# Performance work log

Hardware: AMD Instinct MI355X
Metric: run time of the kernel (lower is better)

## Reference

```python
import jax, jax.numpy as jnp
import numpy as np

THETA = 10000.0

def apply_rope(x, positions):
    # x: [B, H, S, d_k], positions: [S] int
    d_k = x.shape[-1]
    inv_freq = THETA ** (-jnp.arange(0, d_k, 2, dtype=jnp.float32) / d_k)  # [d_k/2]
    ang = positions.astype(jnp.float32)[:, None] * inv_freq[None, :]        # [S, d_k/2]
    cos, sin = jnp.cos(ang), jnp.sin(ang)
    x_even = x[..., 0::2]
    x_odd = x[..., 1::2]
    r_even = x_even * cos - x_odd * sin
    r_odd = x_even * sin + x_odd * cos
    # interleave back
    return jnp.stack([r_even, r_odd], axis=-1).reshape(x.shape)

def setup_inputs() -> dict:
    key = jax.random.key(0)
    k1, k2, k3 = jax.random.split(key, 3)
    B, S, D = 2, 2048, 1024
    x = jax.random.normal(k1, (B, S, D), dtype=jnp.float32)
    token_positions = jnp.arange(S, dtype=jnp.int32)
    W_qkv = jax.random.normal(k2, (3 * D, D), dtype=jnp.float32) * 0.02
    W_o = jax.random.normal(k3, (D, D), dtype=jnp.float32) * 0.02
    return {"x": x, "token_positions": token_positions, "W_qkv": W_qkv, "W_o": W_o}

def reference(x, token_positions, W_qkv, W_o):
    B, S, D = x.shape
    H = 16
    d_k = D // H
    qkv = jnp.einsum('bsd,ed->bse', x, W_qkv)           # [B, S, 3D]
    q, k, v = jnp.split(qkv, 3, axis=-1)
    def to_heads(t):
        return t.reshape(B, S, H, d_k).transpose(0, 2, 1, 3)  # [B, H, S, d_k]
    hq, hk, hv = to_heads(q), to_heads(k), to_heads(v)
    hq = apply_rope(hq, token_positions)
    hk = apply_rope(hk, token_positions)
    scale = d_k ** -0.5
    scores = jnp.einsum('bhqd,bhkd->bhqk', hq, hk) * scale  # [B, H, S, S]
    causal = jnp.tril(jnp.ones((S, S), dtype=bool))
    scores = jnp.where(causal, scores, -jnp.inf)
    attn = jax.nn.softmax(scores, axis=-1)
    out = jnp.einsum('bhqk,bhkd->bhqd', attn, hv)           # [B, H, S, d_k]
    out = out.transpose(0, 2, 1, 3).reshape(B, S, D)
    return jnp.einsum('bsd,ed->bse', out, W_o)
```

## Files before the change

### kernel.cpp

```cpp
#include <hip/hip_runtime.h>
#include <math.h>

typedef short short8 __attribute__((ext_vector_type(8)));
typedef float f32x4 __attribute__((ext_vector_type(4)));

typedef __attribute__((address_space(1))) const void* as1p;
typedef __attribute__((address_space(3))) void* as3p;

__device__ __forceinline__ unsigned short f2bf(float f) {
    unsigned int u = __float_as_uint(f);
    u += 0x7fffu + ((u >> 16) & 1u);
    return (unsigned short)(u >> 16);
}
__device__ __forceinline__ float bf2f(unsigned int bits) {
    return __uint_as_float(bits << 16);
}

__global__ void cvt_all_bf16(const float* __restrict__ x,
                             const float* __restrict__ wqkv,
                             const float* __restrict__ wo,
                             unsigned short* __restrict__ xb,
                             unsigned short* __restrict__ wqkvb,
                             unsigned short* __restrict__ wob) {
    int i = blockIdx.x * blockDim.x + threadIdx.x;
    const float* src;
    unsigned short* dst;
    int off;
    if (i < 1048576)       { src = x;    dst = xb;    off = i; }
    else if (i < 1835008)  { src = wqkv; dst = wqkvb; off = i - 1048576; }
    else                   { src = wo;   dst = wob;   off = i - 1835008; }
    float4 v = ((const float4*)src)[off];
    ushort4 o = make_ushort4(f2bf(v.x), f2bf(v.y), f2bf(v.z), f2bf(v.w));
    ((ushort4*)dst)[off] = o;
}

template <int RF, bool BF16_OUT>
__global__ __launch_bounds__(256) void gemm_nt_mfma(
    const unsigned short* __restrict__ A, const unsigned short* __restrict__ B,
    void* __restrict__ Cv, int N, int K) {
    constexpr int BM = RF * 32;
    __shared__ unsigned short As[BM * 32];
    __shared__ unsigned short Bs[128 * 32];
    const int tid = threadIdx.x;
    const int wave = tid >> 6, lane = tid & 63;
    const int m0 = blockIdx.y * BM, n0 = blockIdx.x << 7;
    const int wr = ((wave >> 1) & 1) * (RF * 16);
    const int wc = (wave & 1) << 6;

    const int r0 = tid >> 2, ko = (tid & 3) << 3;
    const unsigned short* Ap0 = A + (size_t)(m0 + r0) * K + ko;
    const unsigned short* Ap1 = A + (size_t)(m0 + (RF == 4 ? 64 : 0) + r0) * K + ko;
    const unsigned short* Bp0 = B + (size_t)(n0 + r0) * K + ko;
    const unsigned short* Bp1 = B + (size_t)(n0 + 64 + r0) * K + ko;

    f32x4 acc[RF][4] = {};
    const int lro = lane & 15, g8 = (lane >> 4) << 3;

    for (int k0 = 0; k0 < K; k0 += 32) {
        __syncthreads();
        __builtin_amdgcn_global_load_lds((as1p)(Ap0 + k0), (as3p)(As + tid * 8), 16, 0, 0);
        if constexpr (RF == 4)
            __builtin_amdgcn_global_load_lds((as1p)(Ap1 + k0), (as3p)(As + (256 + tid) * 8), 16, 0, 0);
        __builtin_amdgcn_global_load_lds((as1p)(Bp0 + k0), (as3p)(Bs + tid * 8), 16, 0, 0);
        __builtin_amdgcn_global_load_lds((as1p)(Bp1 + k0), (as3p)(Bs + (256 + tid) * 8), 16, 0, 0);
        __syncthreads();

        short8 af[RF], bfr[4];
        #pragma unroll
        for (int i = 0; i < RF; i++) af[i] = *(const short8*)&As[(wr + i * 16 + lro) * 32 + g8];
        #pragma unroll
        for (int j = 0; j < 4; j++) bfr[j] = *(const short8*)&Bs[(wc + j * 16 + lro) * 32 + g8];
        #pragma unroll
        for (int i = 0; i < RF; i++)
            #pragma unroll
            for (int j = 0; j < 4; j++)
                acc[i][j] = __builtin_amdgcn_mfma_f32_16x16x32_bf16(af[i], bfr[j], acc[i][j], 0, 0, 0);
    }

    const int row_b = m0 + wr + ((lane >> 4) << 2);
    const int col_b = n0 + wc + lro;
    #pragma unroll
    for (int i = 0; i < RF; i++)
        #pragma unroll
        for (int j = 0; j < 4; j++)
            #pragma unroll
            for (int r = 0; r < 4; r++) {
                size_t idx = (size_t)(row_b + i * 16 + r) * N + (col_b + j * 16);
                if constexpr (BF16_OUT) ((unsigned short*)Cv)[idx] = f2bf(acc[i][j][r]);
                else ((float*)Cv)[idx] = acc[i][j][r];
            }
}

__global__ void rope_bf16(unsigned short* __restrict__ qkv,
                          const int* __restrict__ pos) {
    int p = blockIdx.x * blockDim.x + threadIdx.x;
    if (p >= 4194304) return;
    int t = p >> 10, r2 = p & 1023;
    int sec = r2 >> 9, e2 = r2 & 511;
    int hh = e2 >> 5, i = e2 & 31;
    int s = t & 2047;
    float fpos = (float)pos[s];
    float ang = fpos * exp2f(-(float)i * 0.41524101186092029f);
    float scl = (sec == 0) ? 0.18033688011112042f : 1.0f;
    float c = cosf(ang) * scl, sn = sinf(ang) * scl;
    unsigned int* base = (unsigned int*)(qkv + (size_t)t * 3072 + sec * 1024 + hh * 64 + 2 * i);
    unsigned int w = *base;
    float xe = bf2f(w & 0xffffu), xo = bf2f(w >> 16);
    float re = xe * c - xo * sn;
    float ro = xe * sn + xo * c;
    *base = (unsigned int)f2bf(re) | ((unsigned int)f2bf(ro) << 16);
}

__global__ __launch_bounds__(256) void flash_attn_mfma(
    const unsigned short* __restrict__ qkv, unsigned short* __restrict__ Ows) {
    const int S = 2048, D3 = 3072;
    const int pp = blockIdx.x, h = blockIdx.y, b = blockIdx.z;
    const int tid = threadIdx.x, wave = tid >> 6, lane = tid & 63;
    const int lro = lane & 15, grp = lane >> 4;

    __shared__ __align__(16) unsigned short Qs[64 * 64];
    __shared__ __align__(16) unsigned short Ks[2][64 * 64];
    __shared__ __align__(16) unsigned int   Vp[2][64 * 36];
    __shared__ __align__(16) unsigned short Ps[64 * 80];

    const int sr = tid >> 3;
    const int sc = ((tid & 7) ^ (sr & 7)) << 3;
    const int kp = tid >> 3, vo = (tid & 7) << 3;
    const int vka = (kp >> 1) + ((kp & 1) << 5);
    const int vcol = (((kp >> 2) ^ (tid & 7)) << 2) | (kp & 3);

    const int cq = grp ^ (lro & 7);
    int kof0[4], kof1[4], vbse[4], vq[4];
    #pragma unroll
    for (int nt = 0; nt < 4; nt++) {
        int R = nt * 16 + lro;
        kof0[nt] = R * 64 + cq * 8;
        kof1[nt] = R * 64 + (cq ^ 4) * 8;
        vbse[nt] = R * 36;
        vq[nt] = (grp ^ (R >> 3)) << 2;
    }
    const int aq0o = (wave * 16 + lro) * 64 + cq * 8;
    const int aq1o = (wave * 16 + lro) * 64 + (cq ^ 4) * 8;
    const int apo = (wave * 16 + lro) * 80 + grp * 8;
    const int prow = wave * 16 + grp * 4;

    const unsigned short* kbg = qkv + (size_t)(b * S) * D3 + 1024 + h * 64;
    const unsigned short* vbg = qkv + (size_t)(b * S) * D3 + 2048 + h * 64;

    for (int ph = 0; ph < 2; ph++) {
        const int qt = ph ? 31 - pp : pp;
        const int q0 = qt << 6;
        const int nkt = qt + 1;

        __syncthreads();
        {
            const unsigned short* qs0 = qkv + (size_t)(b * S + q0 + sr) * D3 + h * 64 + sc;
            *(uint4*)&Qs[tid * 8] = *(const uint4*)qs0;
            *(uint4*)&Qs[(tid + 256) * 8] = *(const uint4*)(qs0 + (size_t)32 * D3);
        }
        __builtin_amdgcn_global_load_lds((as1p)(kbg + (size_t)sr * D3 + sc),
                                         (as3p)&Ks[0][tid * 8], 16, 0, 0);
        __builtin_amdgcn_global_load_lds((as1p)(kbg + (size_t)(sr + 32) * D3 + sc),
                                         (as3p)&Ks[0][(tid + 256) * 8], 16, 0, 0);
        {
            const unsigned short* vs = vbg + (size_t)vka * D3 + vo;
            uint4 va = *(const uint4*)vs;
            uint4 vb = *(const uint4*)(vs + (size_t)16 * D3);
            const unsigned short* pa = (const unsigned short*)&va;
            const unsigned short* pb = (const unsigned short*)&vb;
            #pragma unroll
            for (int j = 0; j < 8; j++)
                Vp[0][(vo + j) * 36 + vcol] = (unsigned)pa[j] | ((unsigned)pb[j] << 16);
        }
        __syncthreads();

        f32x4 acc_o[4] = {};
        float lsum[4] = {0.f, 0.f, 0.f, 0.f};
        short8 aq0 = *(const short8*)&Qs[aq0o];
        short8 aq1 = *(const short8*)&Qs[aq1o];

        for (int kt = 0; kt < nkt; kt++) {
            const int cur = kt & 1, nxt = cur ^ 1;
            const bool pf = (kt + 1 < nkt);
            uint4 va, vb;
            if (pf) {
                const unsigned short* kb1 = kbg + (size_t)((kt + 1) * 64) * D3;
                __builtin_amdgcn_global_load_lds((as1p)(kb1 + (size_t)sr * D3 + sc),
                                                 (as3p)&Ks[nxt][tid * 8], 16, 0, 0);
                __builtin_amdgcn_global_load_lds((as1p)(kb1 + (size_t)(sr + 32) * D3 + sc),
                                                 (as3p)&Ks[nxt][(tid + 256) * 8], 16, 0, 0);
                const unsigned short* vs = vbg + (size_t)((kt + 1) * 64 + vka) * D3 + vo;
                va = *(const uint4*)vs;
                vb = *(const uint4*)(vs + (size_t)16 * D3);
            }

            f32x4 s[4] = {};
            #pragma unroll
            for (int nt = 0; nt < 4; nt++) {
                short8 bk0 = *(const short8*)&Ks[cur][kof0[nt]];
                short8 bk1 = *(const short8*)&Ks[cur][kof1[nt]];
                s[nt] = __builtin_amdgcn_mfma_f32_16x16x32_bf16(aq0, bk0, s[nt], 0, 0, 0);
                s[nt] = __builtin_amdgcn_mfma_f32_16x16x32_bf16(aq1, bk1, s[nt], 0, 0, 0);
            }

            const bool diag = (kt == nkt - 1);
            #pragma unroll
            for (int r = 0; r < 4; r++) {
                float v0 = s[0][r], v1 = s[1][r], v2 = s[2][r], v3 = s[3][r];
                if (diag) {
                    int rowl = prow + r;
                    if (lro > rowl) v0 = -1e30f;
                    if (16 + lro > rowl) v1 = -1e30f;
                    if (32 + lro > rowl) v2 = -1e30f;
                    if (48 + lro > rowl) v3 = -1e30f;
                }
                float p0 = __builtin_amdgcn_exp2f(v0);
                float p1 = __builtin_amdgcn_exp2f(v1);
                float p2 = __builtin_amdgcn_exp2f(v2);
                float p3 = __builtin_amdgcn_exp2f(v3);
                lsum[r] += (p0 + p1) + (p2 + p3);
                unsigned u0 = __float_as_uint(p0) + 0x8000u;
                unsigned u1 = __float_as_uint(p1) + 0x8000u;
                unsigned u2 = __float_as_uint(p2) + 0x8000u;
                unsigned u3 = __float_as_uint(p3) + 0x8000u;
                uint2 w = make_uint2((u0 >> 16) | (u1 & 0xffff0000u),
                                     (u2 >> 16) | (u3 & 0xffff0000u));
                *(uint2*)&Ps[(prow + r) * 80 + lro * 4] = w;
            }

            short8 ap0 = *(const short8*)&Ps[apo];
            short8 ap1 = *(const short8*)&Ps[apo + 32];
            #pragma unroll
            for (int nt = 0; nt < 4; nt++) {
                short8 bv0 = *(const short8*)&Vp[cur][vbse[nt] + vq[nt]];
                short8 bv1 = *(const short8*)&Vp[cur][vbse[nt] + (vq[nt] ^ 16)];
                acc_o[nt] = __builtin_amdgcn_mfma_f32_16x16x32_bf16(ap0, bv0, acc_o[nt], 0, 0, 0);
                acc_o[nt] = __builtin_amdgcn_mfma_f32_16x16x32_bf16(ap1, bv1, acc_o[nt], 0, 0, 0);
            }

            if (pf) {
                const unsigned short* pa = (const unsigned short*)&va;
                const unsigned short* pb = (const unsigned short*)&vb;
                #pragma unroll
                for (int j = 0; j < 8; j++)
                    Vp[nxt][(vo + j) * 36 + vcol] = (unsigned)pa[j] | ((unsigned)pb[j] << 16);
            }
            __syncthreads();
        }

        #pragma unroll
        for (int r = 0; r < 4; r++) {
            float rsum = lsum[r];
            #pragma unroll
            for (int off = 1; off < 16; off <<= 1)
                rsum += __shfl_xor(rsum, off, 16);
            float inv = 1.0f / rsum;
            int row = q0 + prow + r;
            #pragma unroll
            for (int nt = 0; nt < 4; nt++)
                Ows[(size_t)(b * S + row) * 1024 + h * 64 + nt * 16 + lro] =
                    f2bf(acc_o[nt][r] * inv);
        }
    }
}

extern "C" void kernel_launch(void* const* d_in, const int* in_sizes, int n_in,
                              void* d_out, int out_size, void* d_ws, size_t ws_size,
                              hipStream_t stream) {
    const float* x    = (const float*)d_in[0];
    const int*   pos  = (const int*)d_in[1];
    const float* Wqkv = (const float*)d_in[2];
    const float* Wo   = (const float*)d_in[3];
    float* out = (float*)d_out;

    unsigned short* xb    = (unsigned short*)d_ws;
    unsigned short* Wqkvb = xb + (size_t)4096 * 1024;
    unsigned short* Wob   = Wqkvb + (size_t)3072 * 1024;
    unsigned short* qkvb  = Wob + (size_t)1024 * 1024;
    unsigned short* Owsb  = qkvb + (size_t)4096 * 3072;

    cvt_all_bf16<<<8192, 256, 0, stream>>>(x, Wqkv, Wo, xb, Wqkvb, Wob);

    gemm_nt_mfma<4, true><<<dim3(24, 32), 256, 0, stream>>>(xb, Wqkvb, qkvb, 3072, 1024);

    rope_bf16<<<16384, 256, 0, stream>>>(qkvb, pos);

    flash_attn_mfma<<<dim3(16, 16, 2), 256, 0, stream>>>(qkvb, Owsb);

    gemm_nt_mfma<2, false><<<dim3(8, 64), 256, 0, stream>>>(Owsb, Wob, out, 1024, 1024);
}
```

Baseline: 201.1 us.

## Fuse RoPE into QKV GEMM epilogue and remap attention blocks across XCDs

Removes the standalone RoPE kernel and applies the rotation (and the Q scale) inside the QKV GEMM epilogue on fp32 accumulators, using lane shuffles to get each pair partner and hardware sin/cos on range-reduced revolutions. This drops one kernel launch and a full read/write pass over the Q and K parts of the bf16 qkv buffer, and rotates before the bf16 rounding. Separately, the flash-attention block index is remapped so that blocks sharing the same (batch, head) land on the same XCD, which should improve L2 reuse of K/V. The cost is extra epilogue ALU and shuffle work in the GEMM, and a small accuracy risk from the low-precision hardware trig.

```diff
diff --git a/kernel.cpp b/kernel.cpp
--- a/kernel.cpp
+++ b/kernel.cpp
@@ -34,10 +34,10 @@
     ((ushort4*)dst)[off] = o;
 }
 
-template <int RF, bool BF16_OUT>
+template <int RF, bool BF16_OUT, bool DO_ROPE>
 __global__ __launch_bounds__(256) void gemm_nt_mfma(
     const unsigned short* __restrict__ A, const unsigned short* __restrict__ B,
-    void* __restrict__ Cv, int N, int K) {
+    void* __restrict__ Cv, const int* __restrict__ pos, int N, int K) {
     constexpr int BM = RF * 32;
     __shared__ unsigned short As[BM * 32];
     __shared__ unsigned short Bs[128 * 32];
@@ -79,6 +79,38 @@
 
     const int row_b = m0 + wr + ((lane >> 4) << 2);
     const int col_b = n0 + wc + lro;
+
+    if constexpr (DO_ROPE) {
+        const int sec = (n0 + wc) >> 10;
+        if (sec < 2) {
+            const float qs = (sec == 0) ? 0.18033688011112042f : 1.0f;
+            const float sgn = (lane & 1) ? 1.0f : -1.0f;
+            float ps[RF * 4];
+            #pragma unroll
+            for (int i = 0; i < RF; i++)
+                #pragma unroll
+                for (int r = 0; r < 4; r++)
+                    ps[i * 4 + r] = (float)pos[(row_b + i * 16 + r) & 2047];
+            #pragma unroll
+            for (int j = 0; j < 4; j++) {
+                float invf_rev = exp2f(-(float)((lro >> 1) + 8 * j) * 0.41524101186092029f)
+                                 * 0.15915494309189535f;
+                #pragma unroll
+                for (int i = 0; i < RF; i++)
+                    #pragma unroll
+                    for (int r = 0; r < 4; r++) {
+                        float rev = ps[i * 4 + r] * invf_rev;
+                        rev -= floorf(rev);
+                        float c = __builtin_amdgcn_cosf(rev) * qs;
+                        float s = __builtin_amdgcn_sinf(rev) * (qs * sgn);
+                        float mine = acc[i][j][r];
+                        float partner = __shfl_xor(mine, 1, 64);
+                        acc[i][j][r] = mine * c + partner * s;
+                    }
+            }
+        }
+    }
+
     #pragma unroll
     for (int i = 0; i < RF; i++)
         #pragma unroll
@@ -91,30 +123,14 @@
             }
 }
 
-__global__ void rope_bf16(unsigned short* __restrict__ qkv,
-                          const int* __restrict__ pos) {
-    int p = blockIdx.x * blockDim.x + threadIdx.x;
-    if (p >= 4194304) return;
-    int t = p >> 10, r2 = p & 1023;
-    int sec = r2 >> 9, e2 = r2 & 511;
-    int hh = e2 >> 5, i = e2 & 31;
-    int s = t & 2047;
-    float fpos = (float)pos[s];
-    float ang = fpos * exp2f(-(float)i * 0.41524101186092029f);
-    float scl = (sec == 0) ? 0.18033688011112042f : 1.0f;
-    float c = cosf(ang) * scl, sn = sinf(ang) * scl;
-    unsigned int* base = (unsigned int*)(qkv + (size_t)t * 3072 + sec * 1024 + hh * 64 + 2 * i);
-    unsigned int w = *base;
-    float xe = bf2f(w & 0xffffu), xo = bf2f(w >> 16);
-    float re = xe * c - xo * sn;
-    float ro = xe * sn + xo * c;
-    *base = (unsigned int)f2bf(re) | ((unsigned int)f2bf(ro) << 16);
-}
-
 __global__ __launch_bounds__(256) void flash_attn_mfma(
     const unsigned short* __restrict__ qkv, unsigned short* __restrict__ Ows) {
     const int S = 2048, D3 = 3072;
-    const int pp = blockIdx.x, h = blockIdx.y, b = blockIdx.z;
+    const int L = blockIdx.x + (blockIdx.y << 4) + (blockIdx.z << 8);
+    const int xcd = L & 7, t = L >> 3;
+    const int pp = t & 15;
+    const int g2 = xcd + ((t >> 4) << 3);
+    const int h = g2 & 15, b = g2 >> 4;
     const int tid = threadIdx.x, wave = tid >> 6, lane = tid & 63;
     const int lro = lane & 15, grp = lane >> 4;
 
@@ -281,11 +297,11 @@
 
     cvt_all_bf16<<<8192, 256, 0, stream>>>(x, Wqkv, Wo, xb, Wqkvb, Wob);
 
-    gemm_nt_mfma<4, true><<<dim3(24, 32), 256, 0, stream>>>(xb, Wqkvb, qkvb, 3072, 1024);
-
-    rope_bf16<<<16384, 256, 0, stream>>>(qkvb, pos);
+    gemm_nt_mfma<4, true, true><<<dim3(24, 32), 256, 0, stream>>>(
+        xb, Wqkvb, qkvb, pos, 3072, 1024);
 
     flash_attn_mfma<<<dim3(16, 16, 2), 256, 0, stream>>>(qkvb, Owsb);
 
-    gemm_nt_mfma<2, false><<<dim3(8, 64), 256, 0, stream>>>(Owsb, Wob, out, 1024, 1024);
-}
+    gemm_nt_mfma<2, false, false><<<dim3(8, 64), 256, 0, stream>>>(
+        Owsb, Wob, out, nullptr, 1024, 1024);
+}
```

Measured after the change: 186.5 us. 1.08x faster.
